# Performance work log

Hardware: AMD Instinct MI355X
Metric: run time of the kernel (lower is better)

Reference implementation:

```python
import jax, jax.numpy as jnp
import numpy as np

N, D, C, R, O = 256, 64, 32, 16, 32  # batch, features, in-channels (left=right), repetitions, out-channels


def setup_inputs() -> dict:
    key = jax.random.key(0)
    k1, k2, k3 = jax.random.split(key, 3)
    left_ll = jax.random.normal(k1, (N, D, C, R), dtype=jnp.float32)
    right_ll = jax.random.normal(k2, (N, D, C, R), dtype=jnp.float32)
    logits = jax.random.normal(k3, (D, O, R, C, C), dtype=jnp.float32)
    return {"left_ll": left_ll, "right_ll": right_ll, "logits": logits}


def reference(left_ll, right_ll, logits):
    # Normalized weights: softmax over flattened (i, j) channel-pair axis.
    f, co, r, i, j = logits.shape
    weights = jax.nn.softmax(logits.reshape(f, co, r, i * j), axis=-1).reshape(f, co, r, i, j)

    # LogEinsumExp trick: subtract per-(feature, rep) channel max, exponentiate,
    # contract in linear space, then return to log space.
    left_max = jnp.max(left_ll, axis=2, keepdims=True)    # (N, D, 1, R)
    right_max = jnp.max(right_ll, axis=2, keepdims=True)  # (N, D, 1, R)
    left_prob = jnp.exp(left_ll - left_max)
    right_prob = jnp.exp(right_ll - right_max)

    # (N, D, O, R) weighted cross-product over left/right channels.
    prob = jnp.einsum('ndir,ndjr,dorij->ndor', left_prob, right_prob, weights)
    return jnp.log(prob) + left_max + right_max  # maxes broadcast over out-channel axis
```

## Files before the change

### kernel.cpp

```cpp
#include <hip/hip_runtime.h>

#define N_ 256
#define D_ 64
#define C_ 32
#define R_ 16
#define O_ 32

typedef _Float16 half8 __attribute__((ext_vector_type(8)));
typedef _Float16 half4 __attribute__((ext_vector_type(4)));
typedef float f32x16 __attribute__((ext_vector_type(16)));

__global__ __launch_bounds__(256) void prep_kernel(
    const float* __restrict__ left, const float* __restrict__ right,
    _Float16* __restrict__ lw, _Float16* __restrict__ rw,
    float* __restrict__ msum) {
  const int b = blockIdx.x, t = threadIdx.x;
  const int n = ((b >> 3) << 1) | (t >> 7);
  const int d = ((b & 7) << 3) | ((t >> 4) & 7);
  const int r = t & 15;
  const size_t sbase = ((size_t)(n * D_ + d) * C_) * R_ + r;
  const size_t dbase = (size_t)((d * R_ + r) * N_ + n) * C_;

  float lmx = -1e30f, rmx = -1e30f;
  {
    float vals[C_];
#pragma unroll
    for (int i = 0; i < C_; i++) {
      float v = left[sbase + (size_t)i * R_];
      vals[i] = v;
      lmx = fmaxf(lmx, v);
    }
    half8 pk[4];
#pragma unroll
    for (int i = 0; i < C_; i++) pk[i >> 3][i & 7] = (_Float16)__expf(vals[i] - lmx);
    half8* dst = (half8*)(lw + dbase);
#pragma unroll
    for (int q = 0; q < 4; q++) dst[q] = pk[q];
  }
  {
    float vals[C_];
#pragma unroll
    for (int i = 0; i < C_; i++) {
      float v = right[sbase + (size_t)i * R_];
      vals[i] = v;
      rmx = fmaxf(rmx, v);
    }
    half8 pk[4];
#pragma unroll
    for (int i = 0; i < C_; i++) pk[i >> 3][i & 7] = (_Float16)__expf(vals[i] - rmx);
    half8* dst = (half8*)(rw + dbase);
#pragma unroll
    for (int q = 0; q < 4; q++) dst[q] = pk[q];
  }
  msum[(d * R_ + r) * N_ + n] = lmx + rmx;
}

__global__ __launch_bounds__(512, 4) void main_kernel(
    const float* __restrict__ logits, const _Float16* lw, const _Float16* rw,
    const float* __restrict__ msum, float* scrA, float* scrB) {
  __shared__ __align__(16) _Float16 Wl[64 * 64 * 8];
  __shared__ float psum_o[32];
  __shared__ float msum_s[N_];

  const int bid = blockIdx.x;
  const int workid = ((bid & 7) << 7) | (bid >> 3);
  const int d = workid >> 4, r = workid & 15;

  const int t = threadIdx.x;
  const int w = t >> 6, l = t & 63;
  const int o = l & 31, jb = l >> 5;

  const _Float16* lbase = lw + (size_t)((d * R_ + r) * N_) * C_;
  const _Float16* rbase = rw + (size_t)((d * R_ + r) * N_) * C_;
  const int row = (w << 5) | o;
  const half8* lp = (const half8*)(lbase + row * C_ + (jb << 4));
  const half8 LhA = lp[0];
  const half8 LhB = lp[1];
  const half8* rp2 = (const half8*)(rbase + row * C_);
  half8 Rh[4];
#pragma unroll
  for (int q = 0; q < 4; q++) Rh[q] = rp2[q];

  if (t < N_) msum_s[t] = msum[(d * R_ + r) * N_ + t];

  float lsum[4] = {0.f, 0.f, 0.f, 0.f};
#pragma unroll
  for (int hp = 0; hp < 2; hp++) {
    float4 v[2][4];
#pragma unroll
    for (int sp = 0; sp < 2; sp++) {
      const int sl = (hp << 1) | sp;
      const int oa = (w << 2) | sl;
      const float4* lg4 =
          (const float4*)(logits + ((size_t)((d * O_ + oa) * R_ + r) << 10));
#pragma unroll
      for (int k = 0; k < 4; k++) v[sp][k] = lg4[(k << 6) + l];
    }
#pragma unroll
    for (int sp = 0; sp < 2; sp++) {
      const int sl = (hp << 1) | sp;
      const int oa = (w << 2) | sl;
#pragma unroll
      for (int k = 0; k < 4; k++) {
        const float4 f = v[sp][k];
        const float e0 = __expf(f.x), e1 = __expf(f.y), e2 = __expf(f.z),
                    e3 = __expf(f.w);
        lsum[sl] += (e0 + e1) + (e2 + e3);
        half4 hq = {(_Float16)e0, (_Float16)e1, (_Float16)e2, (_Float16)e3};
        const int s_ = ((((k & 1) << 3) | (l >> 3)) << 2) | ((l & 7) >> 1);
        const int slot_ = ((k >> 1) << 5) | oa;
        const int byte_ =
            ((s_ << 10) | (slot_ << 4) | ((l & 1) << 3)) ^ ((s_ & 7) << 4);
        *(half4*)((char*)Wl + byte_) = hq;
      }
    }
  }
#pragma unroll
  for (int sl = 0; sl < 4; sl++) {
    float ss = lsum[sl];
#pragma unroll
    for (int off = 32; off >= 1; off >>= 1) ss += __shfl_xor(ss, off);
    if (l == 0) psum_o[(w << 2) | sl] = ss;
  }
  __syncthreads();

  const float rlogsum = __logf(psum_o[o]);

  f32x16 acc;
#pragma unroll
  for (int g = 0; g < 16; g++) acc[g] = 0.f;

#pragma unroll
  for (int s = 0; s < 64; s++) {
    const int byte_r = ((s << 10) | (l << 4)) ^ ((s & 7) << 4);
    const half8 Bf = *(const half8*)((const char*)Wl + byte_r);
    const int ig = s >> 2;
    const _Float16 Lsc = (ig < 8) ? LhA[ig & 7] : LhB[ig & 7];
    const half8 Ld = {Lsc, Lsc, Lsc, Lsc, Lsc, Lsc, Lsc, Lsc};
    acc = __builtin_amdgcn_mfma_f32_32x32x16_f16(Ld * Rh[s & 3], Bf, acc, 0, 0, 0);
  }

  float* sb = ((w < 4) ? scrA : scrB) + ((size_t)(d * R_ + r) << 12) +
              (((w & 3) << 5) << 5) + o;
#pragma unroll
  for (int g = 0; g < 16; g++) {
    const int rowt = (g & 3) + ((g >> 2) << 3) + (jb << 2);
    const int n = (w << 5) | rowt;
    const float val = __logf(acc[g]) - rlogsum + msum_s[n];
    sb[rowt << 5] = val;
  }
}

__global__ __launch_bounds__(256) void trans_kernel(const float* scrA,
                                                    const float* scrB,
                                                    float* __restrict__ out) {
  __shared__ float tile[8 * 32 * 20];
  const int bid = blockIdx.x;
  const int d = bid >> 5, chunk = bid & 31;
  const int n0 = chunk << 3;
  const float* src = (chunk < 16) ? scrA : scrB;
  const int t = threadIdx.x;

  {
    const int r_t = t >> 4, i16 = t & 15;
    const float* rb =
        src + ((size_t)(d * R_ + r_t) << 12) + (((chunk & 15) << 3) << 5);
#pragma unroll
    for (int k = 0; k < 4; k++) {
      const int f = (k << 4) | i16;
      const float4 v = *(const float4*)(rb + (f << 2));
      const int nl = f >> 3, o4 = (f & 7) << 2;
#pragma unroll
      for (int j = 0; j < 4; j++)
        tile[((nl << 5) | (o4 + j)) * 20 + r_t] = v[j];
    }
  }
  __syncthreads();
  {
    const int n_w = t >> 5, pos = t & 31;
    float* ob = out + (((size_t)(n0 + n_w) * D_ + d) << 9);
#pragma unroll
    for (int k = 0; k < 4; k++) {
      const int idx = (k << 5) | pos;
      const float4 v =
          *(const float4*)&tile[((n_w << 5) | (idx >> 2)) * 20 + ((pos & 3) << 2)];
      *(float4*)(ob + (idx << 2)) = v;
    }
  }
}

extern "C" void kernel_launch(void* const* d_in, const int* in_sizes, int n_in,
                              void* d_out, int out_size, void* d_ws, size_t ws_size,
                              hipStream_t stream) {
  const float* left = (const float*)d_in[0];
  const float* right = (const float*)d_in[1];
  const float* logits = (const float*)d_in[2];
  float* out = (float*)d_out;
  _Float16* lw = (_Float16*)d_ws;
  _Float16* rw = (_Float16*)((char*)d_ws + (size_t)16 * 1024 * 1024);
  float* ms = (float*)((char*)d_ws + (size_t)32 * 1024 * 1024);
  float* scrA = (float*)d_ws;
  float* scrB = (float*)((char*)d_ws + (size_t)16 * 1024 * 1024);

  prep_kernel<<<1024, 256, 0, stream>>>(left, right, lw, rw, ms);
  main_kernel<<<1024, 512, 0, stream>>>(logits, lw, rw, ms, scrA, scrB);
  trans_kernel<<<2048, 256, 0, stream>>>(scrA, scrB, out);
}
```

Before: 275.6 us.

## Split softmax weight staging into two halves and store intermediate log-probs in fp16

The main kernel now stages the exponentiated logits into LDS in two halves of the channel-pair axis. It loads the second half's logits into registers while running the MFMA loop on the first half, then overwrites the same LDS buffer. This halves the LDS footprint, so the launch bound can allow 6 blocks per CU instead of 4, and it overlaps global loads with matrix math. Separately, the intermediate scratch written by the main kernel and read by the transpose kernel switches from fp32 to fp16, halving that round-trip traffic. The cost is an extra barrier and reduced precision of the final log outputs.

```diff
diff --git a/kernel.cpp b/kernel.cpp
--- a/kernel.cpp
+++ b/kernel.cpp
@@ -55,10 +55,10 @@
   msum[(d * R_ + r) * N_ + n] = lmx + rmx;
 }
 
-__global__ __launch_bounds__(512, 4) void main_kernel(
+__global__ __launch_bounds__(512, 6) void main_kernel(
     const float* __restrict__ logits, const _Float16* lw, const _Float16* rw,
-    const float* __restrict__ msum, float* scrA, float* scrB) {
-  __shared__ __align__(16) _Float16 Wl[64 * 64 * 8];
+    const float* __restrict__ msum, _Float16* scrA, _Float16* scrB) {
+  __shared__ __align__(16) _Float16 Wl[32 * 64 * 8];
   __shared__ float psum_o[32];
   __shared__ float msum_s[N_];
 
@@ -83,36 +83,71 @@
 
   if (t < N_) msum_s[t] = msum[(d * R_ + r) * N_ + t];
 
+  const float4* lg4 =
+      (const float4*)(logits + ((size_t)((d * O_ + (w << 2)) * R_ + r) << 10));
+  const int s_loc = ((l >> 3) << 2) | ((l & 7) >> 1);
+  const int wbase = (s_loc << 10) | ((l & 1) << 3);
+  const int wxor = (s_loc & 7) << 4;
+
   float lsum[4] = {0.f, 0.f, 0.f, 0.f};
-#pragma unroll
-  for (int hp = 0; hp < 2; hp++) {
-    float4 v[2][4];
-#pragma unroll
-    for (int sp = 0; sp < 2; sp++) {
-      const int sl = (hp << 1) | sp;
-      const int oa = (w << 2) | sl;
-      const float4* lg4 =
-          (const float4*)(logits + ((size_t)((d * O_ + oa) * R_ + r) << 10));
-#pragma unroll
-      for (int k = 0; k < 4; k++) v[sp][k] = lg4[(k << 6) + l];
-    }
-#pragma unroll
-    for (int sp = 0; sp < 2; sp++) {
-      const int sl = (hp << 1) | sp;
-      const int oa = (w << 2) | sl;
-#pragma unroll
-      for (int k = 0; k < 4; k++) {
-        const float4 f = v[sp][k];
-        const float e0 = __expf(f.x), e1 = __expf(f.y), e2 = __expf(f.z),
-                    e3 = __expf(f.w);
-        lsum[sl] += (e0 + e1) + (e2 + e3);
-        half4 hq = {(_Float16)e0, (_Float16)e1, (_Float16)e2, (_Float16)e3};
-        const int s_ = ((((k & 1) << 3) | (l >> 3)) << 2) | ((l & 7) >> 1);
-        const int slot_ = ((k >> 1) << 5) | oa;
-        const int byte_ =
-            ((s_ << 10) | (slot_ << 4) | ((l & 1) << 3)) ^ ((s_ & 7) << 4);
-        *(half4*)((char*)Wl + byte_) = hq;
-      }
+
+  float4 v[4][2];
+#pragma unroll
+  for (int sl = 0; sl < 4; sl++) {
+#pragma unroll
+    for (int kk = 0; kk < 2; kk++)
+      v[sl][kk] = lg4[(sl << 12) + ((kk << 1) << 6) + l];
+  }
+
+#pragma unroll
+  for (int sl = 0; sl < 4; sl++) {
+    const int oa = (w << 2) | sl;
+#pragma unroll
+    for (int kk = 0; kk < 2; kk++) {
+      const float4 f = v[sl][kk];
+      const float e0 = __expf(f.x), e1 = __expf(f.y), e2 = __expf(f.z),
+                  e3 = __expf(f.w);
+      lsum[sl] += (e0 + e1) + (e2 + e3);
+      half4 hq = {(_Float16)e0, (_Float16)e1, (_Float16)e2, (_Float16)e3};
+      const int slot_ = (kk << 5) | oa;
+      *(half4*)((char*)Wl + ((wbase | (slot_ << 4)) ^ wxor)) = hq;
+    }
+  }
+  __syncthreads();
+
+#pragma unroll
+  for (int sl = 0; sl < 4; sl++) {
+#pragma unroll
+    for (int kk = 0; kk < 2; kk++)
+      v[sl][kk] = lg4[(sl << 12) + (((kk << 1) | 1) << 6) + l];
+  }
+
+  f32x16 acc;
+#pragma unroll
+  for (int g = 0; g < 16; g++) acc[g] = 0.f;
+
+#pragma unroll
+  for (int s = 0; s < 32; s++) {
+    const half8 Bf =
+        *(const half8*)((const char*)Wl + (((s << 10) | (l << 4)) ^ ((s & 7) << 4)));
+    const _Float16 Lsc = LhA[s >> 2];
+    const half8 Ld = {Lsc, Lsc, Lsc, Lsc, Lsc, Lsc, Lsc, Lsc};
+    acc = __builtin_amdgcn_mfma_f32_32x32x16_f16(Ld * Rh[s & 3], Bf, acc, 0, 0, 0);
+  }
+  __syncthreads();
+
+#pragma unroll
+  for (int sl = 0; sl < 4; sl++) {
+    const int oa = (w << 2) | sl;
+#pragma unroll
+    for (int kk = 0; kk < 2; kk++) {
+      const float4 f = v[sl][kk];
+      const float e0 = __expf(f.x), e1 = __expf(f.y), e2 = __expf(f.z),
+                  e3 = __expf(f.w);
+      lsum[sl] += (e0 + e1) + (e2 + e3);
+      half4 hq = {(_Float16)e0, (_Float16)e1, (_Float16)e2, (_Float16)e3};
+      const int slot_ = (kk << 5) | oa;
+      *(half4*)((char*)Wl + ((wbase | (slot_ << 4)) ^ wxor)) = hq;
     }
   }
 #pragma unroll
@@ -124,55 +159,50 @@
   }
   __syncthreads();
 
-  const float rlogsum = __logf(psum_o[o]);
-
-  f32x16 acc;
-#pragma unroll
-  for (int g = 0; g < 16; g++) acc[g] = 0.f;
-
-#pragma unroll
-  for (int s = 0; s < 64; s++) {
-    const int byte_r = ((s << 10) | (l << 4)) ^ ((s & 7) << 4);
-    const half8 Bf = *(const half8*)((const char*)Wl + byte_r);
-    const int ig = s >> 2;
-    const _Float16 Lsc = (ig < 8) ? LhA[ig & 7] : LhB[ig & 7];
+#pragma unroll
+  for (int s = 0; s < 32; s++) {
+    const half8 Bf =
+        *(const half8*)((const char*)Wl + (((s << 10) | (l << 4)) ^ ((s & 7) << 4)));
+    const _Float16 Lsc = LhB[s >> 2];
     const half8 Ld = {Lsc, Lsc, Lsc, Lsc, Lsc, Lsc, Lsc, Lsc};
     acc = __builtin_amdgcn_mfma_f32_32x32x16_f16(Ld * Rh[s & 3], Bf, acc, 0, 0, 0);
   }
 
-  float* sb = ((w < 4) ? scrA : scrB) + ((size_t)(d * R_ + r) << 12) +
-              (((w & 3) << 5) << 5) + o;
+  const float rlogsum = __logf(psum_o[o]);
+
+  _Float16* sb = ((w < 4) ? scrA : scrB) + ((size_t)(d * R_ + r) << 13) +
+                 ((w & 3) << 10) + o;
 #pragma unroll
   for (int g = 0; g < 16; g++) {
     const int rowt = (g & 3) + ((g >> 2) << 3) + (jb << 2);
     const int n = (w << 5) | rowt;
     const float val = __logf(acc[g]) - rlogsum + msum_s[n];
-    sb[rowt << 5] = val;
-  }
-}
-
-__global__ __launch_bounds__(256) void trans_kernel(const float* scrA,
-                                                    const float* scrB,
+    sb[rowt << 5] = (_Float16)val;
+  }
+}
+
+__global__ __launch_bounds__(256) void trans_kernel(const _Float16* scrA,
+                                                    const _Float16* scrB,
                                                     float* __restrict__ out) {
   __shared__ float tile[8 * 32 * 20];
   const int bid = blockIdx.x;
   const int d = bid >> 5, chunk = bid & 31;
   const int n0 = chunk << 3;
-  const float* src = (chunk < 16) ? scrA : scrB;
+  const _Float16* src = (chunk < 16) ? scrA : scrB;
   const int t = threadIdx.x;
 
   {
     const int r_t = t >> 4, i16 = t & 15;
-    const float* rb =
-        src + ((size_t)(d * R_ + r_t) << 12) + (((chunk & 15) << 3) << 5);
+    const _Float16* rb =
+        src + ((size_t)(d * R_ + r_t) << 13) + ((chunk & 15) << 8);
 #pragma unroll
     for (int k = 0; k < 4; k++) {
       const int f = (k << 4) | i16;
-      const float4 v = *(const float4*)(rb + (f << 2));
+      const half4 v = *(const half4*)(rb + (f << 2));
       const int nl = f >> 3, o4 = (f & 7) << 2;
 #pragma unroll
       for (int j = 0; j < 4; j++)
-        tile[((nl << 5) | (o4 + j)) * 20 + r_t] = v[j];
+        tile[((nl << 5) | (o4 + j)) * 20 + r_t] = (float)v[j];
     }
   }
   __syncthreads();
@@ -199,8 +229,8 @@
   _Float16* lw = (_Float16*)d_ws;
   _Float16* rw = (_Float16*)((char*)d_ws + (size_t)16 * 1024 * 1024);
   float* ms = (float*)((char*)d_ws + (size_t)32 * 1024 * 1024);
-  float* scrA = (float*)d_ws;
-  float* scrB = (float*)((char*)d_ws + (size_t)16 * 1024 * 1024);
+  _Float16* scrA = (_Float16*)d_ws;
+  _Float16* scrB = (_Float16*)((char*)d_ws + (size_t)16 * 1024 * 1024);
 
   prep_kernel<<<1024, 256, 0, stream>>>(left, right, lw, rw, ms);
   main_kernel<<<1024, 512, 0, stream>>>(logits, lw, rw, ms, scrA, scrB);
```

Measured after the change: 309.1 us. 1.12x slower.
